# Optimization experiments

Measured on AMD Instinct MI355X. Metric: run time of the kernel, lower is better.

## Reference

```python
import jax, jax.numpy as jnp
import numpy as np

IN_FEATURES = 16384
OUT_FEATURES = 16384
NNZ = 1_000_000
BATCH = 256


def setup_inputs() -> dict:
    key = jax.random.key(0)
    k_x, k_w, k_b, k_r, k_c = jax.random.split(key, 5)
    x = jax.random.normal(k_x, (BATCH, IN_FEATURES), dtype=jnp.float32)
    weight_vals = jax.random.normal(k_w, (NNZ,), dtype=jnp.float32)
    bias = jax.random.normal(k_b, (OUT_FEATURES,), dtype=jnp.float32)
    rows = jax.random.randint(k_r, (NNZ,), 0, OUT_FEATURES, dtype=jnp.int32)
    cols = jax.random.randint(k_c, (NNZ,), 0, IN_FEATURES, dtype=jnp.int32)
    return {"x": x, "weight_vals": weight_vals, "bias": bias,
            "rows": rows, "cols": cols}


def reference(x, weight_vals, bias, rows, cols):
    # SparseLinear forward: y = x @ W^T + b, with W sparse COO of shape
    # [out_features, in_features]; (rows, cols) are W's nnz coordinates.
    # Per-edge contribution: x[:, col] * W[row, col], scattered into out[:, row].
    contrib = x[:, cols] * weight_vals  # [B, nnz]
    # segment-sum edges into output features: [nnz, B] -> [out, B]
    out = jax.ops.segment_sum(contrib.T, rows, num_segments=OUT_FEATURES).T
    return out + bias  # [B, out_features]
```

## Files before the change

kernel.cpp:

```cpp
#include <hip/hip_runtime.h>
#include <hip/hip_bf16.h>
#include <hip/hip_fp16.h>

#define IN_F    16384
#define OUT_F   16384
#define CAP     128
#define NBUCK   512
#define CAPB    2560
#define EPB     2048
#define TBLK    1024

typedef unsigned int u32x4 __attribute__((ext_vector_type(4)));
typedef float f32x4 __attribute__((ext_vector_type(4)));


__global__ void prep_kernel(const float* __restrict__ x,
                            __hip_bfloat16* __restrict__ xTh,
                            const int* __restrict__ rows,
                            const int* __restrict__ cols,
                            const float* __restrict__ vals, int nnz,
                            int* __restrict__ gcursor,
                            uint2* __restrict__ staging) {
    __shared__ int smem[64 * 65];
    int t = threadIdx.x;
    if (blockIdx.x < TBLK) {
        float* tile = (float*)smem;
        int bid = blockIdx.x;
        int i0 = (bid & 255) * 64;
        int b0 = (bid >> 8) * 64;
        int tx4 = t & 15;
        int r16 = t >> 4;
#pragma unroll
        for (int k = 0; k < 4; ++k) {
            int row = r16 + k * 16;
            f32x4 v = *(const f32x4*)(x + (size_t)(b0 + row) * IN_F + i0 + tx4 * 4);
            tile[row * 65 + tx4 * 4 + 0] = v.x;
            tile[row * 65 + tx4 * 4 + 1] = v.y;
            tile[row * 65 + tx4 * 4 + 2] = v.z;
            tile[row * 65 + tx4 * 4 + 3] = v.w;
        }
        __syncthreads();
        int tx = t & 63, ty = t >> 6;
        int h = b0 >> 7, j0 = b0 & 127;
#pragma unroll
        for (int k = 0; k < 64; k += 4) {
            int col = i0 + ty + k;
            xTh[((size_t)h * IN_F + col) * 128 + j0 + tx] =
                __float2bfloat16(tile[tx * 65 + ty + k]);
        }
    } else {
        int* hist = smem;
        int* base = smem + NBUCK;
        hist[t] = 0; hist[t + 256] = 0;
        __syncthreads();
        int i0 = (blockIdx.x - TBLK) * EPB;
        unsigned int pack[8], vb[8];
        int bk[8];
#pragma unroll
        for (int k = 0; k < 8; ++k) {
            int i = i0 + k * 256 + t;
            if (i < nnz) {
                int r = rows[i], c = cols[i];
                pack[k] = ((unsigned int)r << 14) | (unsigned int)c;
                __half hv = __float2half(vals[i]);
                vb[k] = ((unsigned int)c << 16) |
                        (unsigned int)__half_as_ushort(hv);
                bk[k] = r >> 5;
                atomicAdd(&hist[bk[k]], 1);
            } else bk[k] = -1;
        }
        __syncthreads();
#pragma unroll
        for (int q = 0; q < 2; ++q) {
            int bin = t + q * 256;
            int h = hist[bin];
            base[bin] = (h > 0) ? atomicAdd(&gcursor[bin], h) : 0;
        }
        __syncthreads();
        hist[t] = 0; hist[t + 256] = 0;
        __syncthreads();
#pragma unroll
        for (int k = 0; k < 8; ++k) {
            if (bk[k] >= 0) {
                int p = base[bk[k]] + atomicAdd(&hist[bk[k]], 1);
                if (p < CAPB)
                    staging[(size_t)bk[k] * CAPB + p] = make_uint2(pack[k], vb[k]);
            }
        }
    }
}


__global__ void __launch_bounds__(512, 4)
accum_kernel(const unsigned int* __restrict__ xh0,
             const uint2* __restrict__ staging,
             const int* __restrict__ gcursor,
             const float* __restrict__ bias,
             float* __restrict__ out) {
    __shared__ union {
        unsigned int lbin[32 * CAP];
        float slab[32 * 129];
    } u;
    __shared__ int lcnt[32];
    int blk = blockIdx.x;
    int h = blk & 1;
    int bu = blk >> 1;
    int o0 = bu * 32;
    int t = threadIdx.x;
    int w = t >> 6, lane = t & 63;
    {
        u32x4 z = {0u, 0u, 0u, 0u};
#pragma unroll
        for (int i = 0; i < 2; ++i)
            *(u32x4*)&u.lbin[(t + i * 512) * 4] = z;
    }
    if (t < 32) lcnt[t] = 0;
    __syncthreads();
    int n = gcursor[bu];
    if (n > CAPB) n = CAPB;
    const uint2* st = staging + (size_t)bu * CAPB;
    for (int i = t; i < n; i += 512) {
        uint2 r2 = st[i];
        int rl = (r2.x >> 14) & 31;
        int p = atomicAdd(&lcnt[rl], 1);
        if (p < CAP) u.lbin[rl * CAP + p] = r2.y;
    }
    __syncthreads();
    const unsigned int* xh = xh0 + (size_t)h * IN_F * 64;
    float aa[4], ab[4];
#pragma unroll
    for (int pp = 0; pp < 2; ++pp) {
        int rlA = w * 4 + pp * 2;
        int rlB = rlA + 1;
        int cA = lcnt[rlA]; if (cA > CAP) cA = CAP;
        int cB = lcnt[rlB]; if (cB > CAP) cB = CAP;
        int cm = cA > cB ? cA : cB;
        int lim = (cm + 3) & ~3;
        const u32x4* lbA = (const u32x4*)&u.lbin[rlA * CAP];
        const u32x4* lbB = (const u32x4*)&u.lbin[rlB * CAP];
        float a0 = 0.f, a1 = 0.f, b0 = 0.f, b1 = 0.f;
        if (lim > 0) {
            u32x4 curA = lbA[0], curB = lbB[0];
            for (int j = 0; j < lim; j += 4) {
                u32x4 nxtA = lbA[(j >> 2) + 1];
                u32x4 nxtB = lbB[(j >> 2) + 1];
                unsigned int eA[4] = {curA.x, curA.y, curA.z, curA.w};
                unsigned int eB[4] = {curB.x, curB.y, curB.z, curB.w};
                unsigned int sA[4], sB[4], gA[4], gB[4];
#pragma unroll
                for (int k = 0; k < 4; ++k) {
                    sA[k] = __builtin_amdgcn_readfirstlane(eA[k]);
                    sB[k] = __builtin_amdgcn_readfirstlane(eB[k]);
                    gA[k] = *(xh + ((sA[k] >> 16) << 6) + lane);
                    gB[k] = *(xh + ((sB[k] >> 16) << 6) + lane);
                }
#pragma unroll
                for (int k = 0; k < 4; ++k) {
                    float vA = __half2float(__ushort_as_half(
                                   (unsigned short)(sA[k] & 0xffffu)));
                    float vB = __half2float(__ushort_as_half(
                                   (unsigned short)(sB[k] & 0xffffu)));
                    a0 += __uint_as_float(gA[k] << 16) * vA;
                    a1 += __uint_as_float(gA[k] & 0xffff0000u) * vA;
                    b0 += __uint_as_float(gB[k] << 16) * vB;
                    b1 += __uint_as_float(gB[k] & 0xffff0000u) * vB;
                }
                curA = nxtA; curB = nxtB;
            }
        }
        aa[pp * 2 + 0] = a0; ab[pp * 2 + 0] = a1;
        aa[pp * 2 + 1] = b0; ab[pp * 2 + 1] = b1;
    }
    __syncthreads();
#pragma unroll
    for (int rr = 0; rr < 4; ++rr) {
        int rl = w * 4 + rr;
        u.slab[rl * 129 + 2 * lane + 0] = aa[rr];
        u.slab[rl * 129 + 2 * lane + 1] = ab[rr];
    }
    __syncthreads();
#pragma unroll
    for (int it = 0; it < 2; ++it) {
        int item = t + it * 512;
        int bl = item >> 3;
        int q = item & 7;
        f32x4 bv = *(const f32x4*)(bias + o0 + q * 4);
        f32x4 v;
        v.x = u.slab[(q * 4 + 0) * 129 + bl] + bv.x;
        v.y = u.slab[(q * 4 + 1) * 129 + bl] + bv.y;
        v.z = u.slab[(q * 4 + 2) * 129 + bl] + bv.z;
        v.w = u.slab[(q * 4 + 3) * 129 + bl] + bv.w;
        __builtin_nontemporal_store(v,
            (f32x4*)(out + (size_t)(h * 128 + bl) * OUT_F + o0 + q * 4));
    }
}

extern "C" void kernel_launch(void* const* d_in, const int* in_sizes, int n_in,
                              void* d_out, int out_size, void* d_ws, size_t ws_size,
                              hipStream_t stream) {
    const float* x     = (const float*)d_in[0];
    const float* wvals = (const float*)d_in[1];
    const float* bias  = (const float*)d_in[2];
    const int*   rows  = (const int*)d_in[3];
    const int*   cols  = (const int*)d_in[4];
    float* out = (float*)d_out;
    int nnz = in_sizes[1];

    const size_t MB = 1024 * 1024;
    char* ws = (char*)d_ws;
    __hip_bfloat16* xTh = (__hip_bfloat16*)(ws);
    uint2* staging = (uint2*)(ws + 8 * MB);
    int*   gcursor = (int*)(ws + 20 * MB);

    (void)hipMemsetAsync(gcursor, 0, NBUCK * sizeof(int), stream);

    int npart = (nnz + EPB - 1) / EPB;
    prep_kernel<<<TBLK + npart, 256, 0, stream>>>(x, xTh, rows, cols, wvals, nnz,
                                                  gcursor, staging);
    accum_kernel<<<NBUCK * 2, 512, 0, stream>>>((const unsigned int*)xTh, staging,
                                                gcursor, bias, out);
}
```

Measured before the change: 134.0 us.

## Locally sort COO partitions in LDS before coalesced staging writes; widen accum gather batches

The partition phase now uses 4096 edges per block and does a prefix scan over bucket histograms. Each block sorts its records by bucket into shared memory, then writes them to staging in contiguous nontemporal runs instead of scattered stores. Partition blocks are moved ahead of the transpose blocks so the atomic-heavy work starts first. The accumulate kernel processes four rows per wave at once (16 gathers in flight), and its launch bound rises to 6 waves. The trade-offs are higher register pressure and more LDS per prep block.

```diff
diff --git a/kernel.cpp b/kernel.cpp
--- a/kernel.cpp
+++ b/kernel.cpp
@@ -7,7 +7,7 @@
 #define CAP     128
 #define NBUCK   512
 #define CAPB    2560
-#define EPB     2048
+#define EPB     4096
 #define TBLK    1024
 
 typedef unsigned int u32x4 __attribute__((ext_vector_type(4)));
@@ -18,14 +18,78 @@
                             __hip_bfloat16* __restrict__ xTh,
                             const int* __restrict__ rows,
                             const int* __restrict__ cols,
-                            const float* __restrict__ vals, int nnz,
+                            const float* __restrict__ vals, int nnz, int npart,
                             int* __restrict__ gcursor,
                             uint2* __restrict__ staging) {
-    __shared__ int smem[64 * 65];
+    __shared__ __align__(16) union {
+        float tile[64 * 65];
+        struct {
+            uint2 recs[EPB];
+            int hist[NBUCK];
+            int lstart[NBUCK];
+            int gbase[NBUCK];
+            int scanbuf[256];
+        } pa;
+    } sm;
     int t = threadIdx.x;
-    if (blockIdx.x < TBLK) {
-        float* tile = (float*)smem;
-        int bid = blockIdx.x;
+    if ((int)blockIdx.x < npart) {
+        sm.pa.hist[t] = 0; sm.pa.hist[t + 256] = 0;
+        __syncthreads();
+        int i0 = blockIdx.x * EPB;
+        unsigned int pk[16], vb[16];
+#pragma unroll
+        for (int k = 0; k < 16; ++k) {
+            int i = i0 + k * 256 + t;
+            if (i < nnz) {
+                int r = rows[i], c = cols[i];
+                pk[k] = ((unsigned int)r << 14) | (unsigned int)c;
+                vb[k] = ((unsigned int)c << 16) |
+                        (unsigned int)__half_as_ushort(__float2half(vals[i]));
+                atomicAdd(&sm.pa.hist[r >> 5], 1);
+            } else pk[k] = 0xffffffffu;
+        }
+        __syncthreads();
+        int h0 = sm.pa.hist[2 * t], h1 = sm.pa.hist[2 * t + 1];
+        sm.pa.scanbuf[t] = h0 + h1;
+        __syncthreads();
+        for (int off = 1; off < 256; off <<= 1) {
+            int add = (t >= off) ? sm.pa.scanbuf[t - off] : 0;
+            __syncthreads();
+            sm.pa.scanbuf[t] += add;
+            __syncthreads();
+        }
+        int excl = sm.pa.scanbuf[t] - (h0 + h1);
+        sm.pa.lstart[2 * t]     = excl;
+        sm.pa.lstart[2 * t + 1] = excl + h0;
+        sm.pa.gbase[2 * t]     = h0 > 0 ? atomicAdd(&gcursor[2 * t], h0) : 0;
+        sm.pa.gbase[2 * t + 1] = h1 > 0 ? atomicAdd(&gcursor[2 * t + 1], h1) : 0;
+        __syncthreads();
+        sm.pa.hist[t] = 0; sm.pa.hist[t + 256] = 0;
+        __syncthreads();
+#pragma unroll
+        for (int k = 0; k < 16; ++k) {
+            if (pk[k] != 0xffffffffu) {
+                int b = pk[k] >> 19;
+                int pos = sm.pa.lstart[b] + atomicAdd(&sm.pa.hist[b], 1);
+                sm.pa.recs[pos] = make_uint2(pk[k], vb[k]);
+            }
+        }
+        __syncthreads();
+        int total = sm.pa.scanbuf[255];
+        for (int j = t; j < total; j += 256) {
+            uint2 rec = sm.pa.recs[j];
+            int b = rec.x >> 19;
+            int gp = sm.pa.gbase[b] + (j - sm.pa.lstart[b]);
+            if (gp < CAPB) {
+                unsigned long long pv =
+                    (unsigned long long)rec.x | ((unsigned long long)rec.y << 32);
+                __builtin_nontemporal_store(pv,
+                    (unsigned long long*)(staging + (size_t)b * CAPB + gp));
+            }
+        }
+    } else {
+        float* tile = (float*)&sm;
+        int bid = blockIdx.x - npart;
         int i0 = (bid & 255) * 64;
         int b0 = (bid >> 8) * 64;
         int tx4 = t & 15;
@@ -48,50 +112,11 @@
             xTh[((size_t)h * IN_F + col) * 128 + j0 + tx] =
                 __float2bfloat16(tile[tx * 65 + ty + k]);
         }
-    } else {
-        int* hist = smem;
-        int* base = smem + NBUCK;
-        hist[t] = 0; hist[t + 256] = 0;
-        __syncthreads();
-        int i0 = (blockIdx.x - TBLK) * EPB;
-        unsigned int pack[8], vb[8];
-        int bk[8];
-#pragma unroll
-        for (int k = 0; k < 8; ++k) {
-            int i = i0 + k * 256 + t;
-            if (i < nnz) {
-                int r = rows[i], c = cols[i];
-                pack[k] = ((unsigned int)r << 14) | (unsigned int)c;
-                __half hv = __float2half(vals[i]);
-                vb[k] = ((unsigned int)c << 16) |
-                        (unsigned int)__half_as_ushort(hv);
-                bk[k] = r >> 5;
-                atomicAdd(&hist[bk[k]], 1);
-            } else bk[k] = -1;
-        }
-        __syncthreads();
-#pragma unroll
-        for (int q = 0; q < 2; ++q) {
-            int bin = t + q * 256;
-            int h = hist[bin];
-            base[bin] = (h > 0) ? atomicAdd(&gcursor[bin], h) : 0;
-        }
-        __syncthreads();
-        hist[t] = 0; hist[t + 256] = 0;
-        __syncthreads();
-#pragma unroll
-        for (int k = 0; k < 8; ++k) {
-            if (bk[k] >= 0) {
-                int p = base[bk[k]] + atomicAdd(&hist[bk[k]], 1);
-                if (p < CAPB)
-                    staging[(size_t)bk[k] * CAPB + p] = make_uint2(pack[k], vb[k]);
-            }
-        }
     }
 }
 
 
-__global__ void __launch_bounds__(512, 4)
+__global__ void __launch_bounds__(512, 6)
 accum_kernel(const unsigned int* __restrict__ xh0,
              const uint2* __restrict__ staging,
              const int* __restrict__ gcursor,
@@ -118,63 +143,66 @@
     __syncthreads();
     int n = gcursor[bu];
     if (n > CAPB) n = CAPB;
-    const uint2* st = staging + (size_t)bu * CAPB;
+    const unsigned long long* st = (const unsigned long long*)(staging + (size_t)bu * CAPB);
     for (int i = t; i < n; i += 512) {
-        uint2 r2 = st[i];
-        int rl = (r2.x >> 14) & 31;
+        unsigned long long v = __builtin_nontemporal_load(st + i);
+        unsigned int rx = (unsigned int)v;
+        unsigned int ry = (unsigned int)(v >> 32);
+        int rl = (rx >> 14) & 31;
         int p = atomicAdd(&lcnt[rl], 1);
-        if (p < CAP) u.lbin[rl * CAP + p] = r2.y;
+        if (p < CAP) u.lbin[rl * CAP + p] = ry;
     }
     __syncthreads();
     const unsigned int* xh = xh0 + (size_t)h * IN_F * 64;
-    float aa[4], ab[4];
-#pragma unroll
-    for (int pp = 0; pp < 2; ++pp) {
-        int rlA = w * 4 + pp * 2;
-        int rlB = rlA + 1;
-        int cA = lcnt[rlA]; if (cA > CAP) cA = CAP;
-        int cB = lcnt[rlB]; if (cB > CAP) cB = CAP;
-        int cm = cA > cB ? cA : cB;
-        int lim = (cm + 3) & ~3;
-        const u32x4* lbA = (const u32x4*)&u.lbin[rlA * CAP];
-        const u32x4* lbB = (const u32x4*)&u.lbin[rlB * CAP];
-        float a0 = 0.f, a1 = 0.f, b0 = 0.f, b1 = 0.f;
-        if (lim > 0) {
-            u32x4 curA = lbA[0], curB = lbB[0];
-            for (int j = 0; j < lim; j += 4) {
-                u32x4 nxtA = lbA[(j >> 2) + 1];
-                u32x4 nxtB = lbB[(j >> 2) + 1];
-                unsigned int eA[4] = {curA.x, curA.y, curA.z, curA.w};
-                unsigned int eB[4] = {curB.x, curB.y, curB.z, curB.w};
-                unsigned int sA[4], sB[4], gA[4], gB[4];
+    int rl0 = w * 4;
+    int c0 = lcnt[rl0 + 0]; if (c0 > CAP) c0 = CAP;
+    int c1 = lcnt[rl0 + 1]; if (c1 > CAP) c1 = CAP;
+    int c2 = lcnt[rl0 + 2]; if (c2 > CAP) c2 = CAP;
+    int c3 = lcnt[rl0 + 3]; if (c3 > CAP) c3 = CAP;
+    int cm01 = c0 > c1 ? c0 : c1;
+    int cm23 = c2 > c3 ? c2 : c3;
+    int cm = cm01 > cm23 ? cm01 : cm23;
+    int lim = (cm + 3) & ~3;
+    const u32x4* lb0 = (const u32x4*)&u.lbin[(rl0 + 0) * CAP];
+    const u32x4* lb1 = (const u32x4*)&u.lbin[(rl0 + 1) * CAP];
+    const u32x4* lb2 = (const u32x4*)&u.lbin[(rl0 + 2) * CAP];
+    const u32x4* lb3 = (const u32x4*)&u.lbin[(rl0 + 3) * CAP];
+    float aa[4] = {0.f, 0.f, 0.f, 0.f};
+    float ab[4] = {0.f, 0.f, 0.f, 0.f};
+    if (lim > 0) {
+        u32x4 cu0 = lb0[0], cu1 = lb1[0], cu2 = lb2[0], cu3 = lb3[0];
+        for (int j = 0; j < lim; j += 4) {
+            int jn = (j >> 2) + 1;
+            u32x4 nx0 = lb0[jn], nx1 = lb1[jn];
+            u32x4 nx2 = lb2[jn], nx3 = lb3[jn];
+            unsigned int e[16] = {cu0.x, cu0.y, cu0.z, cu0.w,
+                                  cu1.x, cu1.y, cu1.z, cu1.w,
+                                  cu2.x, cu2.y, cu2.z, cu2.w,
+                                  cu3.x, cu3.y, cu3.z, cu3.w};
+            unsigned int s[16], g[16];
+#pragma unroll
+            for (int k = 0; k < 16; ++k) {
+                s[k] = __builtin_amdgcn_readfirstlane(e[k]);
+                g[k] = *(xh + ((s[k] >> 16) << 6) + lane);
+            }
+#pragma unroll
+            for (int r = 0; r < 4; ++r) {
 #pragma unroll
                 for (int k = 0; k < 4; ++k) {
-                    sA[k] = __builtin_amdgcn_readfirstlane(eA[k]);
-                    sB[k] = __builtin_amdgcn_readfirstlane(eB[k]);
-                    gA[k] = *(xh + ((sA[k] >> 16) << 6) + lane);
-                    gB[k] = *(xh + ((sB[k] >> 16) << 6) + lane);
+                    int q = r * 4 + k;
+                    float v = __half2float(__ushort_as_half(
+                                  (unsigned short)(s[q] & 0xffffu)));
+                    aa[r] += __uint_as_float(g[q] << 16) * v;
+                    ab[r] += __uint_as_float(g[q] & 0xffff0000u) * v;
                 }
-#pragma unroll
-                for (int k = 0; k < 4; ++k) {
-                    float vA = __half2float(__ushort_as_half(
-                                   (unsigned short)(sA[k] & 0xffffu)));
-                    float vB = __half2float(__ushort_as_half(
-                                   (unsigned short)(sB[k] & 0xffffu)));
-                    a0 += __uint_as_float(gA[k] << 16) * vA;
-                    a1 += __uint_as_float(gA[k] & 0xffff0000u) * vA;
-                    b0 += __uint_as_float(gB[k] << 16) * vB;
-                    b1 += __uint_as_float(gB[k] & 0xffff0000u) * vB;
-                }
-                curA = nxtA; curB = nxtB;
-            }
-        }
-        aa[pp * 2 + 0] = a0; ab[pp * 2 + 0] = a1;
-        aa[pp * 2 + 1] = b0; ab[pp * 2 + 1] = b1;
+            }
+            cu0 = nx0; cu1 = nx1; cu2 = nx2; cu3 = nx3;
+        }
     }
     __syncthreads();
 #pragma unroll
     for (int rr = 0; rr < 4; ++rr) {
-        int rl = w * 4 + rr;
+        int rl = rl0 + rr;
         u.slab[rl * 129 + 2 * lane + 0] = aa[rr];
         u.slab[rl * 129 + 2 * lane + 1] = ab[rr];
     }
@@ -215,8 +243,8 @@
     (void)hipMemsetAsync(gcursor, 0, NBUCK * sizeof(int), stream);
 
     int npart = (nnz + EPB - 1) / EPB;
-    prep_kernel<<<TBLK + npart, 256, 0, stream>>>(x, xTh, rows, cols, wvals, nnz,
-                                                  gcursor, staging);
+    prep_kernel<<<npart + TBLK, 256, 0, stream>>>(x, xTh, rows, cols, wvals, nnz,
+                                                  npart, gcursor, staging);
     accum_kernel<<<NBUCK * 2, 512, 0, stream>>>((const unsigned int*)xTh, staging,
                                                 gcursor, bias, out);
 }
```

Result: no change. 135.4 us (+1.0%).
